# Optimization experiments

Measured on AMD Instinct MI355X. Metric: run time of the kernel, lower is better.

## Reference

```python
import jax, jax.numpy as jnp
import numpy as np

NUM_NODES = 50000

def _gat_conv(x, edge_index, W, a_src, a_dst, b):
    # PyG GATConv, heads=1: h = x W ; e_ij = LeakyReLU(a_src.h_j + a_dst.h_i)
    # softmax over incoming edges of i ; out_i = sum_j alpha_ij h_j + b
    h = x @ W                                  # [N, F]
    src, dst = edge_index[0], edge_index[1]    # edge j->i : src=j, dst=i
    alpha_s = h @ a_src                        # [N]
    alpha_d = h @ a_dst                        # [N]
    e = jax.nn.leaky_relu(alpha_s[src] + alpha_d[dst], negative_slope=0.2)  # [E]
    # segment softmax over destination nodes
    e_max = jax.ops.segment_max(e, dst, num_segments=NUM_NODES)
    e_exp = jnp.exp(e - e_max[dst])
    denom = jax.ops.segment_sum(e_exp, dst, num_segments=NUM_NODES)
    coef = e_exp / denom[dst]                  # [E]
    out = jax.ops.segment_sum(h[src] * coef[:, None], dst, num_segments=NUM_NODES)
    return out + b

def setup_inputs() -> dict:
    key = jax.random.key(0)
    ks = jax.random.split(key, 10)
    N, E, IN, HID, OUT = NUM_NODES, 800000, 256, 256, 128
    x = jax.random.normal(ks[0], (N, IN), dtype=jnp.float32)
    edge_index = jax.random.randint(ks[1], (2, E), 0, N, dtype=jnp.int32)
    def glorot(k, shape):
        lim = float(np.sqrt(6.0 / (shape[0] + shape[-1])))
        return jax.random.uniform(k, shape, jnp.float32, -lim, lim)
    return {
        'x': x,
        'edge_index': edge_index,
        'W1': glorot(ks[2], (IN, HID)),
        'a_src1': glorot(ks[3], (HID,)),
        'a_dst1': glorot(ks[4], (HID,)),
        'b1': jnp.zeros((HID,), jnp.float32),
        'W2': glorot(ks[5], (HID, OUT)),
        'a_src2': glorot(ks[6], (OUT,)),
        'a_dst2': glorot(ks[7], (OUT,)),
        'b2': jnp.zeros((OUT,), jnp.float32),
    }

def reference(x, edge_index, W1, a_src1, a_dst1, b1, W2, a_src2, a_dst2, b2):
    # add self loops once (same edge_index used by both convs)
    ar = jnp.arange(NUM_NODES, dtype=edge_index.dtype)
    ei = jnp.concatenate([edge_index, jnp.stack([ar, ar])], axis=1)
    x1 = _gat_conv(x, ei, W1, a_src1, a_dst1, b1)
    h = jax.nn.relu(x1)          # dropout p=0.3 is identity in eval mode
    x2 = _gat_conv(h, ei, W2, a_src2, a_dst2, b2)
    return (x2, h)
```

## Files before the change

kernel.cpp:

```cpp
#include <hip/hip_runtime.h>
#include <hip/hip_bf16.h>

#define N_NODES 50000
#define E0      800000
#define ETOT    850000

typedef __bf16 bf16x8 __attribute__((ext_vector_type(8)));
typedef float  f32x4  __attribute__((ext_vector_type(4)));
typedef ushort u16x8  __attribute__((ext_vector_type(8)));
union B8 { u16x8 u; bf16x8 b; };

static __device__ __forceinline__ float b2f(ushort u) {
    union { uint u; float f; } x; x.u = ((uint)u) << 16; return x.f;
}
static __device__ __forceinline__ ushort f2bf(float f) {
    uint u = __builtin_bit_cast(uint, f);
    uint r = (u + 0x7FFFu + ((u >> 16) & 1u)) >> 16;
    return (ushort)r;
}


__global__ __launch_bounds__(256) void k_deg(const int* __restrict__ ei, int* __restrict__ deg) {
    int e = blockIdx.x * 256 + threadIdx.x;
    if (e >= ETOT) return;
    int dst = (e < E0) ? ei[E0 + e] : (e - E0);
    atomicAdd(&deg[dst], 1);
}

__global__ __launch_bounds__(256) void k_scan1(const int* __restrict__ deg, int* __restrict__ offs,
                                               int* __restrict__ bsum) {
    __shared__ int buf[256];
    int tid = threadIdx.x;
    int i = blockIdx.x * 256 + tid;
    int v = (i < N_NODES) ? deg[i] : 0;
    buf[tid] = v;
    __syncthreads();
    for (int off = 1; off < 256; off <<= 1) {
        int t = (tid >= off) ? buf[tid - off] : 0;
        __syncthreads();
        buf[tid] += t;
        __syncthreads();
    }
    if (i < N_NODES) offs[i + 1] = buf[tid];
    if (tid == 255) bsum[blockIdx.x] = buf[255];
}

__global__ __launch_bounds__(256) void k_scan2(int* __restrict__ bsum, int nb) {
    __shared__ int buf[256];
    int tid = threadIdx.x;
    int v = (tid < nb) ? bsum[tid] : 0;
    buf[tid] = v;
    __syncthreads();
    for (int off = 1; off < 256; off <<= 1) {
        int t = (tid >= off) ? buf[tid - off] : 0;
        __syncthreads();
        buf[tid] += t;
        __syncthreads();
    }
    if (tid < nb) bsum[tid] = buf[tid] - v;
}

__global__ __launch_bounds__(256) void k_scan3(int* __restrict__ offs, const int* __restrict__ bsum,
                                               int* __restrict__ cursor) {
    int tid = threadIdx.x;
    int i = blockIdx.x * 256 + tid;
    if (i < N_NODES) {
        int v = offs[i + 1] + bsum[blockIdx.x];
        offs[i + 1] = v;
        cursor[i + 1] = v;
    }
    if (i == 0) { offs[0] = 0; cursor[0] = 0; }
}

__global__ __launch_bounds__(256) void k_scatter(const int* __restrict__ ei, int* __restrict__ cursor,
                                                 int* __restrict__ esrc) {
    int e = blockIdx.x * 256 + threadIdx.x;
    if (e >= ETOT) return;
    int src, dst;
    if (e < E0) { src = ei[e]; dst = ei[E0 + e]; }
    else        { src = e - E0; dst = src; }
    int pos = atomicAdd(&cursor[dst], 1);
    esrc[pos] = src;
}

__global__ __launch_bounds__(256) void k_splitT(const float* __restrict__ W, ushort* __restrict__ th,
                                                ushort* __restrict__ tl, int K, int N) {
    int i = blockIdx.x * 256 + threadIdx.x;
    if (i >= K * N) return;
    int n = i / K, k = i - n * K;
    float v = W[(size_t)k * N + n];
    ushort h = f2bf(v);
    th[(size_t)n * K + k] = h;
    tl[(size_t)n * K + k] = f2bf(v - b2f(h));
}

__global__ __launch_bounds__(256) void k_split1(const float* __restrict__ in, ushort* __restrict__ out, int n4) {
    int i = blockIdx.x * 256 + threadIdx.x;
    if (i >= n4) return;
    float4 v = *(const float4*)(in + (size_t)i * 4);
    ushort4 h;
    h.x = f2bf(v.x); h.y = f2bf(v.y); h.z = f2bf(v.z); h.w = f2bf(v.w);
    *(ushort4*)(out + (size_t)i * 4) = h;
}


__global__ __launch_bounds__(256, 2) void k_gemm_mfma(const ushort* __restrict__ Ab,
                                                      const ushort* __restrict__ Bth,
                                                      const ushort* __restrict__ Btl,
                                                      ushort* __restrict__ Cb, int M, int Nn) {
    constexpr int K = 256;
    __shared__ ushort lds[2][2][8][128][8];
    int tid = threadIdx.x;
    int wid = tid >> 6, lane = tid & 63;
    int wr = wid >> 1, wc = wid & 1;
    int bm = blockIdx.x * 128, bn = blockIdx.y * 128;
    int lr = lane & 15, lg = lane >> 4;

    int sa = tid >> 7, scol = tid & 127;
    const ushort* sb = (sa ? Btl : Bth) + (size_t)(bn + scol) * K;

    const ushort* Ap[4];
#pragma unroll
    for (int m = 0; m < 4; ++m) {
        int row = bm + wr * 64 + m * 16 + lr;
        if (row >= M) row = M - 1;
        Ap[m] = Ab + (size_t)row * K + lg * 8;
    }

    f32x4 acc[4][4] = {};
    u16x8 sv[8];
    bf16x8 aH[2][4];

#pragma unroll
    for (int c = 0; c < 8; ++c) sv[c] = *(const u16x8*)(sb + c * 8);
#pragma unroll
    for (int m = 0; m < 4; ++m) {
        aH[0][m] = *(const bf16x8*)(Ap[m]);
        aH[1][m] = *(const bf16x8*)(Ap[m] + 32);
    }
#pragma unroll
    for (int c = 0; c < 8; ++c) *(u16x8*)&lds[0][sa][c][scol][0] = sv[c];
    __syncthreads();

#pragma unroll
    for (int s = 0; s < 8; ++s) {
        const int w = s >> 1, buf = w & 1, kk = s & 1;
        if (kk == 0 && w < 3) {
#pragma unroll
            for (int c = 0; c < 8; ++c) sv[c] = *(const u16x8*)(sb + (w + 1) * 64 + c * 8);
        }
        bf16x8 bh[4], bl[4];
#pragma unroll
        for (int n = 0; n < 4; ++n) {
            int col = wc * 64 + n * 16 + lr;
            B8 th, tl2;
            th.u = *(const u16x8*)&lds[buf][0][kk * 4 + lg][col][0];
            tl2.u = *(const u16x8*)&lds[buf][1][kk * 4 + lg][col][0];
            bh[n] = th.b; bl[n] = tl2.b;
        }
        bf16x8 ah[4];
#pragma unroll
        for (int m = 0; m < 4; ++m) ah[m] = aH[s & 1][m];
        if (s < 6) {
#pragma unroll
            for (int m = 0; m < 4; ++m) aH[s & 1][m] = *(const bf16x8*)(Ap[m] + (s + 2) * 32);
        }
#pragma unroll
        for (int m = 0; m < 4; ++m)
#pragma unroll
            for (int n = 0; n < 4; ++n) {
                acc[m][n] = __builtin_amdgcn_mfma_f32_16x16x32_bf16(ah[m], bh[n], acc[m][n], 0, 0, 0);
                acc[m][n] = __builtin_amdgcn_mfma_f32_16x16x32_bf16(ah[m], bl[n], acc[m][n], 0, 0, 0);
            }
        if (kk == 1 && w < 3) {
#pragma unroll
            for (int c = 0; c < 8; ++c) *(u16x8*)&lds[buf ^ 1][sa][c][scol][0] = sv[c];
            __syncthreads();
        }
    }
#pragma unroll
    for (int m = 0; m < 4; ++m)
#pragma unroll
        for (int r = 0; r < 4; ++r) {
            int row = bm + wr * 64 + m * 16 + lg * 4 + r;
            if (row < M) {
#pragma unroll
                for (int n = 0; n < 4; ++n) {
                    int col = bn + wc * 64 + n * 16 + lr;
                    Cb[(size_t)row * Nn + col] = f2bf(acc[m][n][r]);
                }
            }
        }
}


template <int F>
__global__ __launch_bounds__(256) void k_alpha(const ushort* __restrict__ H, const float* __restrict__ a_src,
                                               const float* __restrict__ a_dst, float* __restrict__ as,
                                               float* __restrict__ ad) {
    int gw = (blockIdx.x * 256 + threadIdx.x) >> 6;
    int lane = threadIdx.x & 63;
    if (gw >= N_NODES) return;
    float s = 0.f, d = 0.f;
    if (F == 256) {
        ushort4 v = *(const ushort4*)(H + (size_t)gw * 256 + lane * 4);
        float4 cs = *(const float4*)(a_src + lane * 4);
        float4 cd = *(const float4*)(a_dst + lane * 4);
        float f0 = b2f(v.x), f1 = b2f(v.y), f2 = b2f(v.z), f3 = b2f(v.w);
        s = f0 * cs.x + f1 * cs.y + f2 * cs.z + f3 * cs.w;
        d = f0 * cd.x + f1 * cd.y + f2 * cd.z + f3 * cd.w;
    } else {
        ushort2 v = *(const ushort2*)(H + (size_t)gw * 128 + lane * 2);
        float2 cs = *(const float2*)(a_src + lane * 2);
        float2 cd = *(const float2*)(a_dst + lane * 2);
        float f0 = b2f(v.x), f1 = b2f(v.y);
        s = f0 * cs.x + f1 * cs.y;
        d = f0 * cd.x + f1 * cd.y;
    }
    for (int o = 32; o; o >>= 1) { s += __shfl_down(s, o); d += __shfl_down(d, o); }
    if (lane == 0) { as[gw] = s; ad[gw] = d; }
}

template <int F, bool RELU, bool WB>
__global__ __launch_bounds__(256) void k_aggf(const int* __restrict__ offs, const int* __restrict__ esrc,
                                              const float* __restrict__ as, const float* __restrict__ ad,
                                              const ushort* __restrict__ H, const float* __restrict__ bias,
                                              float* __restrict__ out, ushort* __restrict__ hb) {
    constexpr int V = F / 64;
    constexpr float THR = 8.f;
    int gw = (blockIdx.x * 256 + threadIdx.x) >> 6;
    int lane = threadIdx.x & 63;
    if (gw >= N_NODES) return;
    int s0 = offs[gw], s1 = offs[gw + 1];
    float adi = ad[gw];
    float m = -1e30f, ssum = 0.f;
    float acc[V] = {};
    int k = s0;
    for (; k + 7 < s1; k += 8) {
        int rr[8];
#pragma unroll
        for (int q = 0; q < 8; ++q) rr[q] = esrc[k + q];
        float ev[8];
#pragma unroll
        for (int q = 0; q < 8; ++q) ev[q] = as[rr[q]];
        float rows[8][V];
#pragma unroll
        for (int q = 0; q < 8; ++q) {
            if (V == 4) {
                ushort4 v = *(const ushort4*)(H + (size_t)rr[q] * F + lane * 4);
                rows[q][0] = b2f(v.x); rows[q][1] = b2f(v.y); rows[q][2] = b2f(v.z); rows[q][3] = b2f(v.w);
            } else {
                ushort2 v = *(const ushort2*)(H + (size_t)rr[q] * F + lane * 2);
                rows[q][0] = b2f(v.x); rows[q][1] = b2f(v.y);
            }
        }
        float em = -1e30f;
#pragma unroll
        for (int q = 0; q < 8; ++q) {
            float e = ev[q] + adi;
            e = e > 0.f ? e : 0.2f * e;
            ev[q] = e;
            em = fmaxf(em, e);
        }
        if (em > m + THR) {
            float sc = __expf(m - em);
            ssum *= sc;
#pragma unroll
            for (int j = 0; j < V; ++j) acc[j] *= sc;
            m = em;
        }
        float w[8];
#pragma unroll
        for (int q = 0; q < 8; ++q) w[q] = __expf(ev[q] - m);
#pragma unroll
        for (int q = 0; q < 8; ++q) ssum += w[q];
#pragma unroll
        for (int j = 0; j < V; ++j) {
            float a = acc[j];
#pragma unroll
            for (int q = 0; q < 8; ++q) a += w[q] * rows[q][j];
            acc[j] = a;
        }
    }
    for (; k + 3 < s1; k += 4) {
        int rr[4];
#pragma unroll
        for (int q = 0; q < 4; ++q) rr[q] = esrc[k + q];
        float ev[4];
#pragma unroll
        for (int q = 0; q < 4; ++q) ev[q] = as[rr[q]];
        float rows[4][V];
#pragma unroll
        for (int q = 0; q < 4; ++q) {
            if (V == 4) {
                ushort4 v = *(const ushort4*)(H + (size_t)rr[q] * F + lane * 4);
                rows[q][0] = b2f(v.x); rows[q][1] = b2f(v.y); rows[q][2] = b2f(v.z); rows[q][3] = b2f(v.w);
            } else {
                ushort2 v = *(const ushort2*)(H + (size_t)rr[q] * F + lane * 2);
                rows[q][0] = b2f(v.x); rows[q][1] = b2f(v.y);
            }
        }
        float em = -1e30f;
#pragma unroll
        for (int q = 0; q < 4; ++q) {
            float e = ev[q] + adi;
            e = e > 0.f ? e : 0.2f * e;
            ev[q] = e;
            em = fmaxf(em, e);
        }
        if (em > m + THR) {
            float sc = __expf(m - em);
            ssum *= sc;
#pragma unroll
            for (int j = 0; j < V; ++j) acc[j] *= sc;
            m = em;
        }
        float w[4];
#pragma unroll
        for (int q = 0; q < 4; ++q) w[q] = __expf(ev[q] - m);
#pragma unroll
        for (int q = 0; q < 4; ++q) ssum += w[q];
#pragma unroll
        for (int j = 0; j < V; ++j) {
            float a = acc[j];
#pragma unroll
            for (int q = 0; q < 4; ++q) a += w[q] * rows[q][j];
            acc[j] = a;
        }
    }
    for (; k < s1; ++k) {
        int r0 = esrc[k];
        float row0[V];
        if (V == 4) {
            ushort4 v0 = *(const ushort4*)(H + (size_t)r0 * F + lane * 4);
            row0[0] = b2f(v0.x); row0[1] = b2f(v0.y); row0[2] = b2f(v0.z); row0[3] = b2f(v0.w);
        } else {
            ushort2 v0 = *(const ushort2*)(H + (size_t)r0 * F + lane * 2);
            row0[0] = b2f(v0.x); row0[1] = b2f(v0.y);
        }
        float e0 = as[r0] + adi; e0 = e0 > 0.f ? e0 : 0.2f * e0;
        if (e0 > m + THR) {
            float sc = __expf(m - e0);
            ssum *= sc;
#pragma unroll
            for (int j = 0; j < V; ++j) acc[j] *= sc;
            m = e0;
        }
        float w0 = __expf(e0 - m);
        ssum += w0;
#pragma unroll
        for (int j = 0; j < V; ++j) acc[j] += w0 * row0[j];
    }
    float inv = 1.f / ssum;
    float r[V];
#pragma unroll
    for (int j = 0; j < V; ++j) {
        r[j] = acc[j] * inv + bias[lane * V + j];
        if (RELU) r[j] = fmaxf(r[j], 0.f);
    }
    if (V == 4) *(float4*)(out + (size_t)gw * F + lane * 4) = make_float4(r[0], r[1], r[2], r[3]);
    else        *(float2*)(out + (size_t)gw * F + lane * 2) = make_float2(r[0], r[1]);
    if constexpr (WB && V == 4) {
        ushort4 h4;
        h4.x = f2bf(r[0]); h4.y = f2bf(r[1]); h4.z = f2bf(r[2]); h4.w = f2bf(r[3]);
        *(ushort4*)(hb + (size_t)gw * F + lane * 4) = h4;
    }
}


static inline size_t al256(size_t x) { return (x + 255) & ~(size_t)255; }

extern "C" void kernel_launch(void* const* d_in, const int* in_sizes, int n_in,
                              void* d_out, int out_size, void* d_ws, size_t ws_size,
                              hipStream_t stream) {
    const float* x   = (const float*)d_in[0];
    const int*   ei  = (const int*)d_in[1];
    const float* W1  = (const float*)d_in[2];
    const float* as1 = (const float*)d_in[3];
    const float* ad1 = (const float*)d_in[4];
    const float* b1  = (const float*)d_in[5];
    const float* W2  = (const float*)d_in[6];
    const float* as2 = (const float*)d_in[7];
    const float* ad2 = (const float*)d_in[8];
    const float* b2  = (const float*)d_in[9];

    float* out_x2 = (float*)d_out;
    float* out_h  = (float*)d_out + (size_t)N_NODES * 128;

    const size_t NM256 = (size_t)N_NODES * 256 * 2;
    char* base = (char*)d_ws;
    size_t off = 0;
    auto take = [&](size_t bytes) { char* p = base + off; off = al256(off + bytes); return p; };

    ushort* h1b  = (ushort*)take(NM256);
    ushort* xb   = (ushort*)take(NM256);
    ushort* hb   = (ushort*)take(NM256);
    ushort* w1th = (ushort*)take(256 * 256 * 2);
    ushort* w1tl = (ushort*)take(256 * 256 * 2);
    ushort* w2th = (ushort*)take(256 * 128 * 2);
    ushort* w2tl = (ushort*)take(256 * 128 * 2);
    float*  asb  = (float*)take(N_NODES * 4);
    float*  adb  = (float*)take(N_NODES * 4);
    int*    deg  = (int*)take(N_NODES * 4);
    int*    offs = (int*)take((N_NODES + 4) * 4);
    int*    curs = (int*)take((N_NODES + 4) * 4);
    int*    bsum = (int*)take(1024);
    int*    esrc = (int*)take((size_t)ETOT * 4);
    (void)ws_size;

    hipMemsetAsync(deg, 0, N_NODES * sizeof(int), stream);

    int nbE = (ETOT + 255) / 256;
    int nbN = (N_NODES + 255) / 256;
    int nbW = (N_NODES * 64 + 255) / 256;

    k_deg<<<nbE, 256, 0, stream>>>(ei, deg);
    k_scan1<<<nbN, 256, 0, stream>>>(deg, offs, bsum);
    k_scan2<<<1, 256, 0, stream>>>(bsum, nbN);
    k_scan3<<<nbN, 256, 0, stream>>>(offs, bsum, curs);
    k_scatter<<<nbE, 256, 0, stream>>>(ei, curs, esrc);

    k_splitT<<<(256 * 256 + 255) / 256, 256, 0, stream>>>(W1, w1th, w1tl, 256, 256);
    k_splitT<<<(256 * 128 + 255) / 256, 256, 0, stream>>>(W2, w2th, w2tl, 256, 128);
    k_split1<<<(N_NODES * 256 / 4 + 255) / 256, 256, 0, stream>>>(x, xb, N_NODES * 256 / 4);

    dim3 g1((N_NODES + 127) / 128, 2), g2((N_NODES + 127) / 128, 1);

    k_gemm_mfma<<<g1, 256, 0, stream>>>(xb, w1th, w1tl, h1b, N_NODES, 256);
    k_alpha<256><<<nbW, 256, 0, stream>>>(h1b, as1, ad1, asb, adb);
    k_aggf<256, true, true><<<nbW, 256, 0, stream>>>(offs, esrc, asb, adb, h1b, b1, out_h, hb);

    ushort* gb = h1b;
    k_gemm_mfma<<<g2, 256, 0, stream>>>(hb, w2th, w2tl, gb, N_NODES, 128);
    k_alpha<128><<<nbW, 256, 0, stream>>>(gb, as2, ad2, asb, adb);
    k_aggf<128, false, false><<<nbW, 256, 0, stream>>>(offs, esrc, asb, adb, gb, b2, out_x2, nullptr);
}
```

Baseline: 297.0 us.

## Fold attention vectors into weights and fuse alpha computation into prep and aggregation

Precomputes W·a_src and W·a_dst so the per-node attention logits for layer 1 come straight from x in the bf16 conversion kernel, and those for layer 2 from the relu output inside the layer-1 aggregation epilogue. This removes both k_alpha launches and their full reads of the hidden feature matrices. The aggregation main loop is also restructured into a two-buffer software pipeline that issues the next 8-edge batch of gathers before processing the current one, to hide gather latency. Logits now come from fp32 inputs instead of bf16-rounded h, which changes numerics slightly. The double buffers raise register pressure, which could lower occupancy.

```diff
diff --git a/kernel.cpp b/kernel.cpp
--- a/kernel.cpp
+++ b/kernel.cpp
@@ -94,13 +94,44 @@
     tl[(size_t)n * K + k] = f2bf(v - b2f(h));
 }
 
-__global__ __launch_bounds__(256) void k_split1(const float* __restrict__ in, ushort* __restrict__ out, int n4) {
-    int i = blockIdx.x * 256 + threadIdx.x;
-    if (i >= n4) return;
-    float4 v = *(const float4*)(in + (size_t)i * 4);
+__global__ __launch_bounds__(256) void k_wvec(const float* __restrict__ W1, const float* __restrict__ s1v,
+                                              const float* __restrict__ d1v, const float* __restrict__ W2,
+                                              const float* __restrict__ s2v, const float* __restrict__ d2v,
+                                              float* __restrict__ w1s, float* __restrict__ w1d,
+                                              float* __restrict__ w2s, float* __restrict__ w2d) {
+    int gw = (blockIdx.x * 256 + threadIdx.x) >> 6;
+    int lane = threadIdx.x & 63;
+    int vec = gw >> 8, kk = gw & 255;
+    float a = 0.f;
+    if (vec == 0)      { for (int n = lane; n < 256; n += 64) a += W1[(size_t)kk * 256 + n] * s1v[n]; }
+    else if (vec == 1) { for (int n = lane; n < 256; n += 64) a += W1[(size_t)kk * 256 + n] * d1v[n]; }
+    else if (vec == 2) { for (int n = lane; n < 128; n += 64) a += W2[(size_t)kk * 128 + n] * s2v[n]; }
+    else               { for (int n = lane; n < 128; n += 64) a += W2[(size_t)kk * 128 + n] * d2v[n]; }
+    for (int o = 32; o; o >>= 1) a += __shfl_down(a, o);
+    if (lane == 0) {
+        if (vec == 0) w1s[kk] = a;
+        else if (vec == 1) w1d[kk] = a;
+        else if (vec == 2) w2s[kk] = a;
+        else w2d[kk] = a;
+    }
+}
+
+__global__ __launch_bounds__(256) void k_prep1(const float* __restrict__ x, const float* __restrict__ w1s,
+                                               const float* __restrict__ w1d, ushort* __restrict__ xb,
+                                               float* __restrict__ as1, float* __restrict__ ad1) {
+    int gw = (blockIdx.x * 256 + threadIdx.x) >> 6;
+    int lane = threadIdx.x & 63;
+    if (gw >= N_NODES) return;
+    float4 v = *(const float4*)(x + (size_t)gw * 256 + lane * 4);
     ushort4 h;
     h.x = f2bf(v.x); h.y = f2bf(v.y); h.z = f2bf(v.z); h.w = f2bf(v.w);
-    *(ushort4*)(out + (size_t)i * 4) = h;
+    *(ushort4*)(xb + (size_t)gw * 256 + lane * 4) = h;
+    float4 cs = *(const float4*)(w1s + lane * 4);
+    float4 cd = *(const float4*)(w1d + lane * 4);
+    float s = v.x * cs.x + v.y * cs.y + v.z * cs.z + v.w * cs.w;
+    float d = v.x * cd.x + v.y * cd.y + v.z * cd.z + v.w * cd.w;
+    for (int o = 32; o; o >>= 1) { s += __shfl_down(s, o); d += __shfl_down(d, o); }
+    if (lane == 0) { as1[gw] = s; ad1[gw] = d; }
 }
 
 
@@ -194,38 +225,50 @@
 }
 
 
-template <int F>
-__global__ __launch_bounds__(256) void k_alpha(const ushort* __restrict__ H, const float* __restrict__ a_src,
-                                               const float* __restrict__ a_dst, float* __restrict__ as,
-                                               float* __restrict__ ad) {
-    int gw = (blockIdx.x * 256 + threadIdx.x) >> 6;
-    int lane = threadIdx.x & 63;
-    if (gw >= N_NODES) return;
-    float s = 0.f, d = 0.f;
-    if (F == 256) {
-        ushort4 v = *(const ushort4*)(H + (size_t)gw * 256 + lane * 4);
-        float4 cs = *(const float4*)(a_src + lane * 4);
-        float4 cd = *(const float4*)(a_dst + lane * 4);
-        float f0 = b2f(v.x), f1 = b2f(v.y), f2 = b2f(v.z), f3 = b2f(v.w);
-        s = f0 * cs.x + f1 * cs.y + f2 * cs.z + f3 * cs.w;
-        d = f0 * cd.x + f1 * cd.y + f2 * cd.z + f3 * cd.w;
-    } else {
-        ushort2 v = *(const ushort2*)(H + (size_t)gw * 128 + lane * 2);
-        float2 cs = *(const float2*)(a_src + lane * 2);
-        float2 cd = *(const float2*)(a_dst + lane * 2);
-        float f0 = b2f(v.x), f1 = b2f(v.y);
-        s = f0 * cs.x + f1 * cs.y;
-        d = f0 * cd.x + f1 * cd.y;
-    }
-    for (int o = 32; o; o >>= 1) { s += __shfl_down(s, o); d += __shfl_down(d, o); }
-    if (lane == 0) { as[gw] = s; ad[gw] = d; }
-}
-
-template <int F, bool RELU, bool WB>
+#define AGG_LOAD(RR, EV, RW, KK) do {                                              \
+    _Pragma("unroll") for (int q = 0; q < 8; ++q) RR[q] = esrc[(KK) + q];          \
+    _Pragma("unroll") for (int q = 0; q < 8; ++q) EV[q] = as[RR[q]];               \
+    _Pragma("unroll") for (int q = 0; q < 8; ++q) {                                \
+        if constexpr (V == 4) {                                                    \
+            ushort4 v = *(const ushort4*)(H + (size_t)RR[q] * F + lane * 4);       \
+            RW[q][0] = b2f(v.x); RW[q][1] = b2f(v.y);                              \
+            RW[q][2] = b2f(v.z); RW[q][3] = b2f(v.w);                              \
+        } else {                                                                   \
+            ushort2 v = *(const ushort2*)(H + (size_t)RR[q] * F + lane * 2);       \
+            RW[q][0] = b2f(v.x); RW[q][1] = b2f(v.y);                              \
+        }                                                                          \
+    }                                                                              \
+} while (0)
+
+#define AGG_PROC(RR, EV, RW) do {                                                  \
+    float em = -1e30f;                                                             \
+    _Pragma("unroll") for (int q = 0; q < 8; ++q) {                                \
+        float e = EV[q] + adi; e = e > 0.f ? e : 0.2f * e;                         \
+        EV[q] = e; em = fmaxf(em, e);                                              \
+    }                                                                              \
+    if (em > m + THR) {                                                            \
+        float sc = __expf(m - em);                                                 \
+        ssum *= sc;                                                                \
+        _Pragma("unroll") for (int j = 0; j < V; ++j) acc[j] *= sc;                \
+        m = em;                                                                    \
+    }                                                                              \
+    float w[8];                                                                    \
+    _Pragma("unroll") for (int q = 0; q < 8; ++q) w[q] = __expf(EV[q] - m);        \
+    _Pragma("unroll") for (int q = 0; q < 8; ++q) ssum += w[q];                    \
+    _Pragma("unroll") for (int j = 0; j < V; ++j) {                                \
+        float a = acc[j];                                                          \
+        _Pragma("unroll") for (int q = 0; q < 8; ++q) a += w[q] * RW[q][j];        \
+        acc[j] = a;                                                                \
+    }                                                                              \
+} while (0)
+
+template <int F, bool RELU, bool WB, bool A2>
 __global__ __launch_bounds__(256) void k_aggf(const int* __restrict__ offs, const int* __restrict__ esrc,
                                               const float* __restrict__ as, const float* __restrict__ ad,
                                               const ushort* __restrict__ H, const float* __restrict__ bias,
-                                              float* __restrict__ out, ushort* __restrict__ hb) {
+                                              float* __restrict__ out, ushort* __restrict__ hb,
+                                              const float* __restrict__ w2s, const float* __restrict__ w2d,
+                                              float* __restrict__ as2, float* __restrict__ ad2) {
     constexpr int V = F / 64;
     constexpr float THR = 8.f;
     int gw = (blockIdx.x * 256 + threadIdx.x) >> 6;
@@ -235,18 +278,33 @@
     float adi = ad[gw];
     float m = -1e30f, ssum = 0.f;
     float acc[V] = {};
+
+    int nb = (s1 - s0) >> 3;
     int k = s0;
-    for (; k + 7 < s1; k += 8) {
-        int rr[8];
-#pragma unroll
-        for (int q = 0; q < 8; ++q) rr[q] = esrc[k + q];
-        float ev[8];
-#pragma unroll
-        for (int q = 0; q < 8; ++q) ev[q] = as[rr[q]];
-        float rows[8][V];
-#pragma unroll
-        for (int q = 0; q < 8; ++q) {
-            if (V == 4) {
+    int rrA[8]; float evA[8]; float rwA[8][V];
+    int rrB[8]; float evB[8]; float rwB[8][V];
+    if (nb > 0) AGG_LOAD(rrA, evA, rwA, k);
+    for (int b = 0; b < nb; ++b) {
+        if ((b & 1) == 0) {
+            if (b + 1 < nb) AGG_LOAD(rrB, evB, rwB, k + 8);
+            AGG_PROC(rrA, evA, rwA);
+        } else {
+            if (b + 1 < nb) AGG_LOAD(rrA, evA, rwA, k + 8);
+            AGG_PROC(rrB, evB, rwB);
+        }
+        k += 8;
+    }
+    for (; k + 3 < s1; k += 4) {
+        int rr[4];
+#pragma unroll
+        for (int q = 0; q < 4; ++q) rr[q] = esrc[k + q];
+        float ev[4];
+#pragma unroll
+        for (int q = 0; q < 4; ++q) ev[q] = as[rr[q]];
+        float rows[4][V];
+#pragma unroll
+        for (int q = 0; q < 4; ++q) {
+            if constexpr (V == 4) {
                 ushort4 v = *(const ushort4*)(H + (size_t)rr[q] * F + lane * 4);
                 rows[q][0] = b2f(v.x); rows[q][1] = b2f(v.y); rows[q][2] = b2f(v.z); rows[q][3] = b2f(v.w);
             } else {
@@ -256,52 +314,6 @@
         }
         float em = -1e30f;
 #pragma unroll
-        for (int q = 0; q < 8; ++q) {
-            float e = ev[q] + adi;
-            e = e > 0.f ? e : 0.2f * e;
-            ev[q] = e;
-            em = fmaxf(em, e);
-        }
-        if (em > m + THR) {
-            float sc = __expf(m - em);
-            ssum *= sc;
-#pragma unroll
-            for (int j = 0; j < V; ++j) acc[j] *= sc;
-            m = em;
-        }
-        float w[8];
-#pragma unroll
-        for (int q = 0; q < 8; ++q) w[q] = __expf(ev[q] - m);
-#pragma unroll
-        for (int q = 0; q < 8; ++q) ssum += w[q];
-#pragma unroll
-        for (int j = 0; j < V; ++j) {
-            float a = acc[j];
-#pragma unroll
-            for (int q = 0; q < 8; ++q) a += w[q] * rows[q][j];
-            acc[j] = a;
-        }
-    }
-    for (; k + 3 < s1; k += 4) {
-        int rr[4];
-#pragma unroll
-        for (int q = 0; q < 4; ++q) rr[q] = esrc[k + q];
-        float ev[4];
-#pragma unroll
-        for (int q = 0; q < 4; ++q) ev[q] = as[rr[q]];
-        float rows[4][V];
-#pragma unroll
-        for (int q = 0; q < 4; ++q) {
-            if (V == 4) {
-                ushort4 v = *(const ushort4*)(H + (size_t)rr[q] * F + lane * 4);
-                rows[q][0] = b2f(v.x); rows[q][1] = b2f(v.y); rows[q][2] = b2f(v.z); rows[q][3] = b2f(v.w);
-            } else {
-                ushort2 v = *(const ushort2*)(H + (size_t)rr[q] * F + lane * 2);
-                rows[q][0] = b2f(v.x); rows[q][1] = b2f(v.y);
-            }
-        }
-        float em = -1e30f;
-#pragma unroll
         for (int q = 0; q < 4; ++q) {
             float e = ev[q] + adi;
             e = e > 0.f ? e : 0.2f * e;
@@ -331,7 +343,7 @@
     for (; k < s1; ++k) {
         int r0 = esrc[k];
         float row0[V];
-        if (V == 4) {
+        if constexpr (V == 4) {
             ushort4 v0 = *(const ushort4*)(H + (size_t)r0 * F + lane * 4);
             row0[0] = b2f(v0.x); row0[1] = b2f(v0.y); row0[2] = b2f(v0.z); row0[3] = b2f(v0.w);
         } else {
@@ -364,6 +376,14 @@
         ushort4 h4;
         h4.x = f2bf(r[0]); h4.y = f2bf(r[1]); h4.z = f2bf(r[2]); h4.w = f2bf(r[3]);
         *(ushort4*)(hb + (size_t)gw * F + lane * 4) = h4;
+    }
+    if constexpr (A2 && V == 4) {
+        float4 cs = *(const float4*)(w2s + lane * 4);
+        float4 cd = *(const float4*)(w2d + lane * 4);
+        float s2 = r[0] * cs.x + r[1] * cs.y + r[2] * cs.z + r[3] * cs.w;
+        float d2 = r[0] * cd.x + r[1] * cd.y + r[2] * cd.z + r[3] * cd.w;
+        for (int o = 32; o; o >>= 1) { s2 += __shfl_down(s2, o); d2 += __shfl_down(d2, o); }
+        if (lane == 0) { as2[gw] = s2; ad2[gw] = d2; }
     }
 }
 
@@ -399,8 +419,14 @@
     ushort* w1tl = (ushort*)take(256 * 256 * 2);
     ushort* w2th = (ushort*)take(256 * 128 * 2);
     ushort* w2tl = (ushort*)take(256 * 128 * 2);
-    float*  asb  = (float*)take(N_NODES * 4);
-    float*  adb  = (float*)take(N_NODES * 4);
+    float*  w1s  = (float*)take(256 * 4);
+    float*  w1d  = (float*)take(256 * 4);
+    float*  w2s  = (float*)take(256 * 4);
+    float*  w2d  = (float*)take(256 * 4);
+    float*  a1s  = (float*)take(N_NODES * 4);
+    float*  a1d  = (float*)take(N_NODES * 4);
+    float*  a2s  = (float*)take(N_NODES * 4);
+    float*  a2d  = (float*)take(N_NODES * 4);
     int*    deg  = (int*)take(N_NODES * 4);
     int*    offs = (int*)take((N_NODES + 4) * 4);
     int*    curs = (int*)take((N_NODES + 4) * 4);
@@ -422,16 +448,18 @@
 
     k_splitT<<<(256 * 256 + 255) / 256, 256, 0, stream>>>(W1, w1th, w1tl, 256, 256);
     k_splitT<<<(256 * 128 + 255) / 256, 256, 0, stream>>>(W2, w2th, w2tl, 256, 128);
-    k_split1<<<(N_NODES * 256 / 4 + 255) / 256, 256, 0, stream>>>(x, xb, N_NODES * 256 / 4);
+    k_wvec<<<256, 256, 0, stream>>>(W1, as1, ad1, W2, as2, ad2, w1s, w1d, w2s, w2d);
+    k_prep1<<<nbW, 256, 0, stream>>>(x, w1s, w1d, xb, a1s, a1d);
 
     dim3 g1((N_NODES + 127) / 128, 2), g2((N_NODES + 127) / 128, 1);
 
     k_gemm_mfma<<<g1, 256, 0, stream>>>(xb, w1th, w1tl, h1b, N_NODES, 256);
-    k_alpha<256><<<nbW, 256, 0, stream>>>(h1b, as1, ad1, asb, adb);
-    k_aggf<256, true, true><<<nbW, 256, 0, stream>>>(offs, esrc, asb, adb, h1b, b1, out_h, hb);
+    k_aggf<256, true, true, true><<<nbW, 256, 0, stream>>>(offs, esrc, a1s, a1d, h1b, b1,
+                                                           out_h, hb, w2s, w2d, a2s, a2d);
 
     ushort* gb = h1b;
     k_gemm_mfma<<<g2, 256, 0, stream>>>(hb, w2th, w2tl, gb, N_NODES, 128);
-    k_alpha<128><<<nbW, 256, 0, stream>>>(gb, as2, ad2, asb, adb);
-    k_aggf<128, false, false><<<nbW, 256, 0, stream>>>(offs, esrc, asb, adb, gb, b2, out_x2, nullptr);
-}
+    k_aggf<128, false, false, false><<<nbW, 256, 0, stream>>>(offs, esrc, a2s, a2d, gb, b2,
+                                                              out_x2, nullptr, nullptr, nullptr,
+                                                              nullptr, nullptr);
+}
```

After: 392.8 us. 32.3% more time.
